# Kernel tuning notes

Hardware: AMD Instinct MI355X
Metric: run time of the kernel (lower is better)

The kernel has to match this reference:

```python
import jax, jax.numpy as jnp
import numpy as np

B, N, C_IN = 8, 8192, 64
M, K, RADIUS = 1024, 64, 0.2   # num_centers, num_neighbors, ball radius
LAYERS = [128, 128, 256]
EPS = 1e-5


def setup_inputs() -> dict:
    key = jax.random.key(0)
    ks = jax.random.split(key, 3 + len(LAYERS))
    feat = jax.random.normal(ks[0], (B, C_IN, N), jnp.float32)
    coords = jax.random.uniform(ks[1], (B, 3, N), jnp.float32)  # unit cube
    cond = jax.random.normal(ks[2], (B, C_IN), jnp.float32)
    params = {}
    c_prev = C_IN + 3  # include_coordinates=True
    for i, c_out in enumerate(LAYERS):
        params[f"w{i}"] = jax.random.normal(ks[3 + i], (c_out, c_prev), jnp.float32) / np.sqrt(c_prev).astype(np.float32)
        params[f"b{i}"] = jnp.zeros((c_out,), jnp.float32)
        params[f"gamma{i}"] = jnp.ones((c_out,), jnp.float32)
        params[f"beta{i}"] = jnp.zeros((c_out,), jnp.float32)
        c_prev = c_out
    return {"feat": feat, "coords": coords, "cond": cond, **params}


def fps(pts, m):
    """Furthest point sampling. pts: (B,N,3) -> (B,m) int32 indices. Starts at index 0."""
    B_, N_, _ = pts.shape

    def step(carry, _):
        dist, far = carry                                   # (B,N), (B,)
        centroid = jnp.take_along_axis(pts, far[:, None, None], axis=1)  # (B,1,3)
        d = jnp.sum((pts - centroid) ** 2, -1)              # (B,N)
        dist = jnp.minimum(dist, d)
        nxt = jnp.argmax(dist, -1).astype(jnp.int32)
        return (dist, nxt), far

    init = (jnp.full((B_, N_), 1e10, jnp.float32), jnp.zeros((B_,), jnp.int32))
    _, idx = jax.lax.scan(step, init, None, length=m)
    return idx.T                                            # (B,m)


def ball_query(pts, centers, radius, k):
    """pts (B,N,3), centers (B,M,3) -> neighbor indices (B,M,k).
    First k in-radius points (original order); empty slots repeat the first hit."""
    d2 = jnp.sum((centers[:, :, None, :] - pts[:, None, :, :]) ** 2, -1)  # (B,M,N)
    within = d2 < radius * radius
    # stable sort keys: valid points (0) first, keeping original point order
    order = jnp.argsort(jnp.where(within, 0, 1).astype(jnp.int32), axis=-1, stable=True)[..., :k]
    cnt = within.sum(-1, keepdims=True)                      # (B,M,1)
    slot = jnp.arange(k)
    return jnp.where(slot < cnt, order, order[..., :1])      # pad with first valid idx


def gather(x, idx):
    """x (B,N,D), idx (B,M,K) -> (B,M,K,D)"""
    return jax.vmap(lambda a, i: a[i])(x, idx)


def reference(feat, coords, cond,
              w0, b0, gamma0, beta0,
              w1, b1, gamma1, beta1,
              w2, b2, gamma2, beta2):
    pts = coords.transpose(0, 2, 1)                          # (B,N,3)
    cidx = fps(pts, M)                                       # (B,M)
    centers = jnp.take_along_axis(pts, cidx[..., None], axis=1)  # (B,M,3)
    nidx = ball_query(pts, centers, RADIUS, K)               # (B,M,K)
    rel = gather(pts, nidx) - centers[:, :, None, :]         # (B,M,K,3) relative coords
    nfeat = gather(feat.transpose(0, 2, 1), nidx)            # (B,M,K,C)
    x = jnp.concatenate([rel, nfeat], axis=-1)               # (B,M,K,3+C), coords first
    # Shared MLP: 1x1 conv + BatchNorm (batch stats) + ReLU per layer
    for w, b, g, be in ((w0, b0, gamma0, beta0), (w1, b1, gamma1, beta1), (w2, b2, gamma2, beta2)):
        x = jnp.einsum('bmkc,oc->bmko', x, w) + b
        mu = x.mean((0, 1, 2))
        var = x.var((0, 1, 2))
        x = (x - mu) * jax.lax.rsqrt(var + EPS) * g + be
        x = jax.nn.relu(x)
    out = x.max(axis=2).transpose(0, 2, 1)                   # max over nsample -> (B,Cout,M)
    return out, centers.transpose(0, 2, 1), cond
```

## Files before the change

### kernel.cpp

```cpp
#include <hip/hip_runtime.h>

#define NB    8
#define NPTS  8192
#define NCTR  1024
#define KNN   64
#define NGRP  8192
#define SAMP  524288
#define EPSB  1e-5f

#define OFF_CIDX 0ull
#define OFF_NIDX 32768ull
#define OFF_SS   2129920ull
#define OFF_PSUM 2134016ull
#define OFF_PSQR 4231168ull
#define OFF_GMAX 6328320ull
#define OFF_GMIN 14716928ull
#define OFF_FT   23105536ull
#define OFF_Y1   31494144ull
#define NEED_BIG 165711872ull

typedef unsigned short ushort8 __attribute__((ext_vector_type(8)));
typedef short short8v __attribute__((ext_vector_type(8)));
typedef float f32x4 __attribute__((ext_vector_type(4)));
typedef float f32x2 __attribute__((ext_vector_type(2)));

__device__ __forceinline__ unsigned short f2b(float f) {
  unsigned int u = __builtin_bit_cast(unsigned int, f);
  u += 0x7fffu + ((u >> 16) & 1u);
  return (unsigned short)(u >> 16);
}
__device__ __forceinline__ float b2f(unsigned short s) {
  unsigned int u = ((unsigned int)s) << 16;
  return __builtin_bit_cast(float, u);
}

template <int CTRL>
__device__ __forceinline__ float dppmax(float x) {
  int m = __builtin_amdgcn_update_dpp(0, __builtin_bit_cast(int, x), CTRL, 0xf, 0xf, true);
  return fmaxf(x, __builtin_bit_cast(float, m));
}

__global__ __launch_bounds__(256) void fps_kernel(const float* __restrict__ coords,
                                                  int* __restrict__ cidx,
                                                  float* __restrict__ centers_out) {
  const int b = blockIdx.x;
  const int t = threadIdx.x;
  const int wid = t >> 6, lane = t & 63;
  __shared__ float4 sc4[NPTS];
  __shared__ unsigned long long red[2][4];
  const float* cb = coords + (size_t)b * 3 * NPTS;
  for (int i = t; i < NPTS; i += 256)
    sc4[i] = make_float4(cb[i], cb[NPTS + i], cb[2 * NPTS + i], 0.f);
  __syncthreads();
  constexpr int PT = NPTS / 256;
  constexpr int P2 = PT / 2;
  f32x2 px[P2], py[P2], pz[P2], dst[P2];
#pragma unroll
  for (int j = 0; j < P2; ++j) {
    int p = t * PT + 2 * j;
    px[j] = (f32x2){cb[p], cb[p + 1]};
    py[j] = (f32x2){cb[NPTS + p], cb[NPTS + p + 1]};
    pz[j] = (f32x2){cb[2 * NPTS + p], cb[2 * NPTS + p + 1]};
    dst[j] = (f32x2){1e10f, 1e10f};
  }
  int cur = 0;
  float4 c0 = sc4[0];
  float cx = c0.x, cy = c0.y, cz = c0.z;
  int parity = 0;
  for (int s = 0; s < NCTR; ++s) {
    if (t == 0) {
      cidx[b * NCTR + s] = cur;
      centers_out[(b * 3 + 0) * NCTR + s] = cx;
      centers_out[(b * 3 + 1) * NCTR + s] = cy;
      centers_out[(b * 3 + 2) * NCTR + s] = cz;
    }
    f32x2 cx2 = {cx, cx}, cy2 = {cy, cy}, cz2 = {cz, cz};
    f32x2 bv2 = {-1.0f, -1.0f};
#pragma unroll
    for (int j = 0; j < P2; ++j) {
#pragma clang fp contract(off)
      f32x2 dx = px[j] - cx2;
      f32x2 dy = py[j] - cy2;
      f32x2 dz = pz[j] - cz2;
      f32x2 d2 = (dx * dx + dy * dy) + dz * dz;
      f32x2 nd = __builtin_elementwise_min(dst[j], d2);
      dst[j] = nd;
      bv2 = __builtin_elementwise_max(bv2, nd);
    }
    float bv = fmaxf(bv2.x, bv2.y);
    float r = bv;
    r = dppmax<0x111>(r);
    r = dppmax<0x112>(r);
    r = dppmax<0x114>(r);
    r = dppmax<0x118>(r);
    r = dppmax<0x142>(r);
    r = dppmax<0x143>(r);
    float wm = __builtin_bit_cast(float,
        __builtin_amdgcn_readlane(__builtin_bit_cast(int, r), 63));
    int li = 0x7fffffff;
#pragma unroll
    for (int j = P2 - 1; j >= 0; --j) {
      if (dst[j].y == wm) li = t * PT + 2 * j + 1;
      if (dst[j].x == wm) li = t * PT + 2 * j;
    }
    unsigned long long mask = __ballot(bv == wm);
    int widx = __shfl(li, (int)__builtin_ctzll(mask));
    if (lane == 0)
      red[parity][wid] =
          ((unsigned long long)__builtin_bit_cast(unsigned int, wm) << 32) |
          (unsigned long long)(~(unsigned int)widx);
    __syncthreads();
    unsigned long long best = red[parity][0];
#pragma unroll
    for (int k = 1; k < 4; ++k) {
      unsigned long long o = red[parity][k];
      best = (o > best) ? o : best;
    }
    cur = (int)(~(unsigned int)best);
    float4 cc = sc4[cur];
    cx = cc.x; cy = cc.y; cz = cc.z;
    parity ^= 1;
  }
}

__global__ __launch_bounds__(256) void featT_kernel(const float* __restrict__ feat,
                                                    unsigned short* __restrict__ fT) {
  int b  = blockIdx.y;
  int j  = blockIdx.x * 64 + (threadIdx.x & 63);
  int cg = threadIdx.x >> 6;
  ushort8 v0, v1;
#pragma unroll
  for (int cc = 0; cc < 8; ++cc)
    v0[cc] = f2b(feat[((size_t)b * 64 + cg * 16 + cc) * NPTS + j]);
#pragma unroll
  for (int cc = 0; cc < 8; ++cc)
    v1[cc] = f2b(feat[((size_t)b * 64 + cg * 16 + 8 + cc) * NPTS + j]);
  unsigned short* dst = fT + ((size_t)b * NPTS + j) * 64 + cg * 16;
  *(ushort8*)dst = v0;
  *(ushort8*)(dst + 8) = v1;
}

__global__ __launch_bounds__(256) void bq_kernel(const float* __restrict__ coords,
                                                 const int* __restrict__ cidx,
                                                 int* __restrict__ nidx) {
  const int b = blockIdx.y;
  const int w = threadIdx.x >> 6, lane = threadIdx.x & 63;
  const int m = blockIdx.x * 4 + w;
  const float* cb = coords + (size_t)b * 3 * NPTS;
  const int cen = cidx[b * NCTR + m];
  const float cx = cb[cen], cy = cb[NPTS + cen], cz = cb[2 * NPTS + cen];
  int* outp = nidx + ((size_t)b * NCTR + m) * KNN;
  const float RR = (float)(0.2 * 0.2);
  int found = 0, first = -1;
  for (int chunk = 0; chunk < NPTS / 64 && found < KNN; ++chunk) {
    int p = chunk * 64 + lane;
    float dx = __fsub_rn(cx, cb[p]);
    float dy = __fsub_rn(cy, cb[NPTS + p]);
    float dz = __fsub_rn(cz, cb[2 * NPTS + p]);
    float d2 = __fadd_rn(__fadd_rn(__fmul_rn(dx, dx), __fmul_rn(dy, dy)), __fmul_rn(dz, dz));
    bool pred = d2 < RR;
    unsigned long long mask = __ballot(pred);
    if (pred) {
      int rank = __popcll(mask & ((1ull << lane) - 1ull));
      int slot = found + rank;
      if (slot < KNN) outp[slot] = p;
    }
    if (first < 0 && mask != 0ull) first = chunk * 64 + __builtin_ctzll(mask);
    found += __popcll(mask);
  }
  if (found < KNN) {
    int f = (first < 0) ? 0 : first;
    if (lane >= found) outp[lane] = f;
  }
}

template <int NL, bool READY1, bool WRITEY1>
__global__ __launch_bounds__(256) void fused_kernel(
    const unsigned short* __restrict__ fT, const float* __restrict__ coords,
    const int* __restrict__ cidx, const int* __restrict__ nidx,
    unsigned short* __restrict__ y1, const float* __restrict__ ss,
    const float* __restrict__ w0, const float* __restrict__ b0,
    const float* __restrict__ w1, const float* __restrict__ b1,
    const float* __restrict__ w2, const float* __restrict__ b2,
    float* __restrict__ psum, float* __restrict__ psqr,
    float* __restrict__ gmax, float* __restrict__ gmin) {
  __shared__ __align__(16) unsigned short Xs[4 * 64 * 128];
  __shared__ __align__(16) unsigned short Wbuf[128 * 128];
  __shared__ float s_bias[128];
  __shared__ float s_sc0[128], s_sh0[128], s_sc1[128], s_sh1[128];
  __shared__ float s_rs[4][128], s_rq[4][128];

  const int t = threadIdx.x;
  const int wg = t >> 6, lane = t & 63;
  const int r16 = lane & 15, kg = lane >> 4;
  const int g = blockIdx.x * 4 + wg;
  const int bb_ = g >> 10;
  const int rsw = lane & 7;
  unsigned short* xrow = &Xs[(wg * 64 + lane) * 128];

  if constexpr (NL >= 2 && !READY1) {
    if (t < 128) { s_sc0[t] = ss[t]; s_sh0[t] = ss[128 + t]; }
  }
  if constexpr (NL >= 3) {
    if (t < 128) { s_sc1[t] = ss[256 + t]; s_sh1[t] = ss[384 + t]; }
  }

  auto stageW = [&](const float* w, const float* bia, bool remap0, int oh) {
    for (int e = t; e < 128 * 128; e += 256) {
      int o = e >> 7, c = e & 127;
      float v;
      if (remap0) {
        int lc = (c < 64) ? (c + 3) : ((c < 67) ? (c - 64) : -1);
        v = (lc >= 0) ? w[o * 67 + lc] : 0.f;
      } else {
        v = w[((size_t)(oh * 128 + o)) * 128 + c];
      }
      Wbuf[(o << 7) + ((((c >> 3) ^ (o & 7)) << 3) | (c & 7))] = f2b(v);
    }
    if (t < 128) s_bias[t] = bia[oh * 128 + t];
  };

  auto statsOut = [&](float (&sv8)[8], float (&sq8)[8], int coff) {
#pragma unroll
    for (int nt = 0; nt < 8; ++nt) {
      sv8[nt] += __shfl_xor(sv8[nt], 16); sv8[nt] += __shfl_xor(sv8[nt], 32);
      sq8[nt] += __shfl_xor(sq8[nt], 16); sq8[nt] += __shfl_xor(sq8[nt], 32);
    }
    if (lane < 16) {
#pragma unroll
      for (int nt = 0; nt < 8; ++nt) {
        s_rs[wg][nt * 16 + lane] = sv8[nt];
        s_rq[wg][nt * 16 + lane] = sq8[nt];
      }
    }
    __syncthreads();
    if (t < 128) {
      float sB = s_rs[0][t] + s_rs[1][t] + s_rs[2][t] + s_rs[3][t];
      float qB = s_rq[0][t] + s_rq[1][t] + s_rq[2][t] + s_rq[3][t];
      psum[(size_t)blockIdx.x * 256 + coff + t] = sB;
      psqr[(size_t)blockIdx.x * 256 + coff + t] = qB;
    }
  };

  short8v a[4][4];

  if constexpr (!READY1) {
    {
      int j = nidx[(size_t)g * KNN + lane];
      int cen = cidx[g];
      const unsigned short* fr = fT + ((size_t)bb_ * NPTS + j) * 64;
#pragma unroll
      for (int ch = 0; ch < 8; ++ch)
        *(ushort8*)(xrow + ((ch ^ rsw) << 3)) = *(const ushort8*)(fr + ch * 8);
      const float* cb = coords + (size_t)bb_ * 3 * NPTS;
      float rx = __fsub_rn(cb[j], cb[cen]);
      float ry = __fsub_rn(cb[NPTS + j], cb[NPTS + cen]);
      float rz = __fsub_rn(cb[2 * NPTS + j], cb[2 * NPTS + cen]);
      ushort8 rv = {f2b(rx), f2b(ry), f2b(rz), 0, 0, 0, 0, 0};
      *(ushort8*)(xrow + ((8 ^ rsw) << 3)) = rv;
      ushort8 zz = {0, 0, 0, 0, 0, 0, 0, 0};
#pragma unroll
      for (int ch = 9; ch < 16; ++ch)
        *(ushort8*)(xrow + ((ch ^ rsw) << 3)) = zz;
    }
    stageW(w0, b0, true, 0);
    __syncthreads();

#pragma unroll
    for (int st = 0; st < 4; ++st) {
      int row = st * 16 + r16;
#pragma unroll
      for (int ks = 0; ks < 3; ++ks)
        a[st][ks] = __builtin_bit_cast(short8v,
            *(const ushort8*)&Xs[(wg * 64 + row) * 128 + (((ks * 4 + kg) ^ (row & 7)) << 3)]);
    }
    {
      float sv8[8], sq8[8];
#pragma unroll
      for (int nt = 0; nt < 8; ++nt) { sv8[nt] = 0.f; sq8[nt] = 0.f; }
#pragma unroll
      for (int nt = 0; nt < 8; ++nt) {
        int o = nt * 16 + r16;
        short8v wb[3];
#pragma unroll
        for (int ks = 0; ks < 3; ++ks)
          wb[ks] = __builtin_bit_cast(short8v,
              *(const ushort8*)&Wbuf[(o << 7) + (((ks * 4 + kg) ^ (o & 7)) << 3)]);
        float bia = s_bias[o];
        float sc = 0.f, sh = 0.f;
        if constexpr (NL >= 2) { sc = s_sc0[o]; sh = s_sh0[o]; }
#pragma unroll
        for (int st = 0; st < 4; ++st) {
          f32x4 acc = {0.f, 0.f, 0.f, 0.f};
#pragma unroll
          for (int ks = 0; ks < 3; ++ks)
            acc = __builtin_amdgcn_mfma_f32_16x16x32_bf16(a[st][ks], wb[ks], acc, 0, 0, 0);
#pragma unroll
          for (int r = 0; r < 4; ++r) {
            float v = acc[r] + bia;
            if constexpr (NL == 1) {
              sv8[nt] += v; sq8[nt] = fmaf(v, v, sq8[nt]);
            } else {
              float x = fmaxf(fmaf(v, sc, sh), 0.f);
              int row = st * 16 + kg * 4 + r;
              Xs[(wg * 64 + row) * 128 + ((((o >> 3) ^ (row & 7)) << 3) | (o & 7))] = f2b(x);
            }
          }
        }
      }
      if constexpr (NL == 1) { statsOut(sv8, sq8, 0); return; }
    }

    if constexpr (NL >= 2) {
      __syncthreads();
      stageW(w1, b1, false, 0);
      __syncthreads();
#pragma unroll
    for (int st = 0; st < 4; ++st) {
        int row = st * 16 + r16;
#pragma unroll
        for (int ks = 0; ks < 4; ++ks)
          a[st][ks] = __builtin_bit_cast(short8v,
              *(const ushort8*)&Xs[(wg * 64 + row) * 128 + (((ks * 4 + kg) ^ (row & 7)) << 3)]);
      }
      float sv8[8], sq8[8];
#pragma unroll
      for (int nt = 0; nt < 8; ++nt) { sv8[nt] = 0.f; sq8[nt] = 0.f; }
#pragma unroll
      for (int nt = 0; nt < 8; ++nt) {
        int o = nt * 16 + r16;
        short8v wb[4];
#pragma unroll
        for (int ks = 0; ks < 4; ++ks)
          wb[ks] = __builtin_bit_cast(short8v,
              *(const ushort8*)&Wbuf[(o << 7) + (((ks * 4 + kg) ^ (o & 7)) << 3)]);
        float bia = s_bias[o];
        float sc = 0.f, sh = 0.f;
        if constexpr (NL >= 3) { sc = s_sc1[o]; sh = s_sh1[o]; }
#pragma unroll
        for (int st = 0; st < 4; ++st) {
          f32x4 acc = {0.f, 0.f, 0.f, 0.f};
#pragma unroll
          for (int ks = 0; ks < 4; ++ks)
            acc = __builtin_amdgcn_mfma_f32_16x16x32_bf16(a[st][ks], wb[ks], acc, 0, 0, 0);
#pragma unroll
          for (int r = 0; r < 4; ++r) {
            float v = acc[r] + bia;
            int row = st * 16 + kg * 4 + r;
            if constexpr (NL == 2) {
              sv8[nt] += v; sq8[nt] = fmaf(v, v, sq8[nt]);
              if constexpr (WRITEY1)
                y1[((size_t)g * 64 + row) * 128 + o] = f2b(v);
            } else {
              float x = fmaxf(fmaf(v, sc, sh), 0.f);
              Xs[(wg * 64 + row) * 128 + ((((o >> 3) ^ (row & 7)) << 3) | (o & 7))] = f2b(x);
            }
          }
        }
      }
      if constexpr (NL == 2) { statsOut(sv8, sq8, 0); return; }
    }
  } else {
    __syncthreads();
    const unsigned short* yr = y1 + ((size_t)g * 64 + lane) * 128;
#pragma unroll
    for (int ch = 0; ch < 16; ++ch) {
      ushort8 vv = *(const ushort8*)(yr + ch * 8);
      ushort8 ov;
#pragma unroll
      for (int jj = 0; jj < 8; ++jj) {
        int c = ch * 8 + jj;
        ov[jj] = f2b(fmaxf(fmaf(b2f(vv[jj]), s_sc1[c], s_sh1[c]), 0.f));
      }
      *(ushort8*)(xrow + ((ch ^ rsw) << 3)) = ov;
    }
  }

  if constexpr (NL == 3) {
#pragma unroll
    for (int st = 0; st < 4; ++st) {
      int row = st * 16 + r16;
#pragma unroll
      for (int ks = 0; ks < 4; ++ks)
        a[st][ks] = __builtin_bit_cast(short8v,
            *(const ushort8*)&Xs[(wg * 64 + row) * 128 + (((ks * 4 + kg) ^ (row & 7)) << 3)]);
    }
    for (int h = 0; h < 2; ++h) {
      __syncthreads();
      stageW(w2, b2, false, h);
      __syncthreads();
      float mx8[8], mn8[8], sv8[8], sq8[8];
#pragma unroll
      for (int nt = 0; nt < 8; ++nt) { mx8[nt] = -1e30f; mn8[nt] = 1e30f; sv8[nt] = 0.f; sq8[nt] = 0.f; }
#pragma unroll
      for (int nt = 0; nt < 8; ++nt) {
        int o = nt * 16 + r16;
        short8v wb[4];
#pragma unroll
        for (int ks = 0; ks < 4; ++ks)
          wb[ks] = __builtin_bit_cast(short8v,
              *(const ushort8*)&Wbuf[(o << 7) + (((ks * 4 + kg) ^ (o & 7)) << 3)]);
        float bia = s_bias[o];
#pragma unroll
        for (int st = 0; st < 4; ++st) {
          f32x4 acc = {0.f, 0.f, 0.f, 0.f};
#pragma unroll
          for (int ks = 0; ks < 4; ++ks)
            acc = __builtin_amdgcn_mfma_f32_16x16x32_bf16(a[st][ks], wb[ks], acc, 0, 0, 0);
#pragma unroll
          for (int r = 0; r < 4; ++r) {
            float v = acc[r] + bia;
            mx8[nt] = fmaxf(mx8[nt], v); mn8[nt] = fminf(mn8[nt], v);
            sv8[nt] += v; sq8[nt] = fmaf(v, v, sq8[nt]);
          }
        }
      }
#pragma unroll
      for (int nt = 0; nt < 8; ++nt) {
        mx8[nt] = fmaxf(mx8[nt], __shfl_xor(mx8[nt], 16));
        mx8[nt] = fmaxf(mx8[nt], __shfl_xor(mx8[nt], 32));
        mn8[nt] = fminf(mn8[nt], __shfl_xor(mn8[nt], 16));
        mn8[nt] = fminf(mn8[nt], __shfl_xor(mn8[nt], 32));
      }
      if (lane < 16) {
#pragma unroll
        for (int nt = 0; nt < 8; ++nt) {
          gmax[(size_t)g * 256 + h * 128 + nt * 16 + lane] = mx8[nt];
          gmin[(size_t)g * 256 + h * 128 + nt * 16 + lane] = mn8[nt];
        }
      }
      statsOut(sv8, sq8, h * 128);
    }
  }
}

template <int O>
__global__ __launch_bounds__(256) void ss_kernel(const float* __restrict__ psum,
                                                 const float* __restrict__ psqr,
                                                 const float* __restrict__ gamma,
                                                 const float* __restrict__ beta,
                                                 float* __restrict__ ss_out) {
  int c = blockIdx.x;
  int t = threadIdx.x;
  float s = 0.f, q = 0.f;
  for (int i = t; i < 2048; i += 256) {
    s += psum[(size_t)i * 256 + c];
    q += psqr[(size_t)i * 256 + c];
  }
  int lane = t & 63, wid = t >> 6;
#pragma unroll
  for (int off = 32; off > 0; off >>= 1) { s += __shfl_down(s, off); q += __shfl_down(q, off); }
  __shared__ float rv[4], rqv[4];
  if (lane == 0) { rv[wid] = s; rqv[wid] = q; }
  __syncthreads();
  if (t == 0) {
    s = rv[0] + rv[1] + rv[2] + rv[3];
    q = rqv[0] + rqv[1] + rqv[2] + rqv[3];
    const float inv = 1.0f / (float)SAMP;
    float mu = s * inv;
    float var = fmaxf(q * inv - mu * mu, 0.f);
    float rs = 1.0f / sqrtf(var + EPSB);
    float sc = gamma[c] * rs;
    ss_out[c] = sc;
    ss_out[O + c] = beta[c] - mu * sc;
  }
}

__global__ __launch_bounds__(256) void final_kernel(const float* __restrict__ gmax,
                                                    const float* __restrict__ gmin,
                                                    const float* __restrict__ ss2,
                                                    float* __restrict__ out) {
  int b = blockIdx.x >> 5, mt = blockIdx.x & 31;
  int t = threadIdx.x;
  __shared__ float tile[32][257];
  float sc = ss2[t], sh = ss2[256 + t];
  size_t base = ((size_t)b * 1024 + mt * 32) * 256;
#pragma unroll
  for (int r = 0; r < 32; ++r) {
    float A = fmaf(gmax[base + r * 256 + t], sc, sh);
    float C = fmaf(gmin[base + r * 256 + t], sc, sh);
    tile[r][t] = fmaxf(fmaxf(A, C), 0.f);
  }
  __syncthreads();
  for (int i = t; i < 8192; i += 256) {
    int o = i >> 5, ml = i & 31;
    out[((size_t)b * 256 + o) * 1024 + mt * 32 + ml] = tile[ml][o];
  }
}

__global__ void cond_kernel(const float* __restrict__ cond, float* __restrict__ dst) {
  dst[threadIdx.x] = cond[threadIdx.x];
}

extern "C" void kernel_launch(void* const* d_in, const int* in_sizes, int n_in,
                              void* d_out, int out_size, void* d_ws, size_t ws_size,
                              hipStream_t stream) {
  const float* feat   = (const float*)d_in[0];
  const float* coords = (const float*)d_in[1];
  const float* cond   = (const float*)d_in[2];
  const float* w0  = (const float*)d_in[3];
  const float* b0  = (const float*)d_in[4];
  const float* ga0 = (const float*)d_in[5];
  const float* be0 = (const float*)d_in[6];
  const float* w1  = (const float*)d_in[7];
  const float* b1  = (const float*)d_in[8];
  const float* ga1 = (const float*)d_in[9];
  const float* be1 = (const float*)d_in[10];
  const float* w2  = (const float*)d_in[11];
  const float* b2  = (const float*)d_in[12];
  const float* ga2 = (const float*)d_in[13];
  const float* be2 = (const float*)d_in[14];

  char* ws = (char*)d_ws;
  int* cidxp = (int*)(ws + OFF_CIDX);
  int* nidxp = (int*)(ws + OFF_NIDX);
  float* ss   = (float*)(ws + OFF_SS);
  float* psum = (float*)(ws + OFF_PSUM);
  float* psqr = (float*)(ws + OFF_PSQR);
  float* gmax = (float*)(ws + OFF_GMAX);
  float* gmin = (float*)(ws + OFF_GMIN);
  unsigned short* fT = (unsigned short*)(ws + OFF_FT);
  unsigned short* y1 = (unsigned short*)(ws + OFF_Y1);

  float* out         = (float*)d_out;
  float* centers_out = out + (size_t)8 * 256 * 1024;
  float* cond_out    = centers_out + (size_t)8 * 3 * 1024;

  const bool big = (ws_size >= NEED_BIG);

  fps_kernel<<<8, 256, 0, stream>>>(coords, cidxp, centers_out);
  featT_kernel<<<dim3(128, 8), 256, 0, stream>>>(feat, fT);
  bq_kernel<<<dim3(256, 8), 256, 0, stream>>>(coords, cidxp, nidxp);

  fused_kernel<1, false, false><<<2048, 256, 0, stream>>>(
      fT, coords, cidxp, nidxp, y1, ss, w0, b0, w1, b1, w2, b2, psum, psqr, gmax, gmin);
  ss_kernel<128><<<128, 256, 0, stream>>>(psum, psqr, ga0, be0, ss);

  if (big) {
    fused_kernel<2, false, true><<<2048, 256, 0, stream>>>(
        fT, coords, cidxp, nidxp, y1, ss, w0, b0, w1, b1, w2, b2, psum, psqr, gmax, gmin);
  } else {
    fused_kernel<2, false, false><<<2048, 256, 0, stream>>>(
        fT, coords, cidxp, nidxp, y1, ss, w0, b0, w1, b1, w2, b2, psum, psqr, gmax, gmin);
  }
  ss_kernel<128><<<128, 256, 0, stream>>>(psum, psqr, ga1, be1, ss + 256);

  if (big) {
    fused_kernel<3, true, false><<<2048, 256, 0, stream>>>(
        fT, coords, cidxp, nidxp, y1, ss, w0, b0, w1, b1, w2, b2, psum, psqr, gmax, gmin);
  } else {
    fused_kernel<3, false, false><<<2048, 256, 0, stream>>>(
        fT, coords, cidxp, nidxp, y1, ss, w0, b0, w1, b1, w2, b2, psum, psqr, gmax, gmin);
  }
  ss_kernel<256><<<256, 256, 0, stream>>>(psum, psqr, ga2, be2, ss + 512);

  final_kernel<<<256, 256, 0, stream>>>(gmax, gmin, ss + 512, out);
  cond_kernel<<<1, 512, 0, stream>>>(cond, cond_out);
}
```

Before: 1.504 ms.

## Spatially bin points in FPS so threads skip distance updates via bbox bound

Sorts each batch's points into an 8x8x8 voxel grid, using a shared-memory counting sort, so each thread owns a spatially compact set of 32 points with a bounding box. On every FPS step a thread compares the box's minimum distance to the new center with its current best min-distance and skips the distance update when no point can change. The per-wave argmax tie-break now goes through a packed original-index key reduced with DPP instead of ballot plus shuffle. This adds a sort prologue and some branch divergence, and relies on keeping the original index order for ties.

```diff
diff --git a/kernel.cpp b/kernel.cpp
--- a/kernel.cpp
+++ b/kernel.cpp
@@ -39,33 +39,90 @@
   int m = __builtin_amdgcn_update_dpp(0, __builtin_bit_cast(int, x), CTRL, 0xf, 0xf, true);
   return fmaxf(x, __builtin_bit_cast(float, m));
 }
+template <int CTRL>
+__device__ __forceinline__ unsigned dppumax(unsigned x) {
+  unsigned m = (unsigned)__builtin_amdgcn_update_dpp(0, (int)x, CTRL, 0xf, 0xf, true);
+  return (x > m) ? x : m;
+}
 
 __global__ __launch_bounds__(256) void fps_kernel(const float* __restrict__ coords,
                                                   int* __restrict__ cidx,
                                                   float* __restrict__ centers_out) {
-  const int b = blockIdx.x;
-  const int t = threadIdx.x;
+  const int b = blockIdx.x, t = threadIdx.x;
   const int wid = t >> 6, lane = t & 63;
-  __shared__ float4 sc4[NPTS];
+  __shared__ float4 pts[NPTS];
+  __shared__ int cnt[512];
+  __shared__ int part[256];
+  __shared__ int cstart[512];
   __shared__ unsigned long long red[2][4];
   const float* cb = coords + (size_t)b * 3 * NPTS;
-  for (int i = t; i < NPTS; i += 256)
-    sc4[i] = make_float4(cb[i], cb[NPTS + i], cb[2 * NPTS + i], 0.f);
-  __syncthreads();
-  constexpr int PT = NPTS / 256;
-  constexpr int P2 = PT / 2;
+
+  cnt[t] = 0; cnt[t + 256] = 0;
+  __syncthreads();
+  for (int i = t; i < NPTS; i += 256) {
+    float x = cb[i], y = cb[NPTS + i], z = cb[2 * NPTS + i];
+    int ix = min(max((int)(x * 8.f), 0), 7);
+    int iy = min(max((int)(y * 8.f), 0), 7);
+    int iz = min(max((int)(z * 8.f), 0), 7);
+    atomicAdd(&cnt[ix + 8 * iy + 64 * iz], 1);
+  }
+  __syncthreads();
+  part[t] = cnt[2 * t] + cnt[2 * t + 1];
+  __syncthreads();
+  for (int off = 1; off < 256; off <<= 1) {
+    int v = (t >= off) ? part[t - off] : 0;
+    __syncthreads();
+    part[t] += v;
+    __syncthreads();
+  }
+  {
+    int e = (t > 0) ? part[t - 1] : 0;
+    cstart[2 * t] = e;
+    cstart[2 * t + 1] = e + cnt[2 * t];
+  }
+  __syncthreads();
+  cnt[t] = 0; cnt[t + 256] = 0;
+  __syncthreads();
+  for (int i = t; i < NPTS; i += 256) {
+    float x = cb[i], y = cb[NPTS + i], z = cb[2 * NPTS + i];
+    int ix = min(max((int)(x * 8.f), 0), 7);
+    int iy = min(max((int)(y * 8.f), 0), 7);
+    int iz = min(max((int)(z * 8.f), 0), 7);
+    int c = ix + 8 * iy + 64 * iz;
+    int r = atomicAdd(&cnt[c], 1);
+    int slot = cstart[c] + r;
+    pts[slot] = make_float4(x, y, z, __builtin_bit_cast(float, i));
+  }
+  __syncthreads();
+
+  constexpr int PT = 32, P2 = 16;
   f32x2 px[P2], py[P2], pz[P2], dst[P2];
+  unsigned noi[PT];
+  float lox = 1e30f, loy = 1e30f, loz = 1e30f;
+  float hix = -1e30f, hiy = -1e30f, hiz = -1e30f;
 #pragma unroll
   for (int j = 0; j < P2; ++j) {
-    int p = t * PT + 2 * j;
-    px[j] = (f32x2){cb[p], cb[p + 1]};
-    py[j] = (f32x2){cb[NPTS + p], cb[NPTS + p + 1]};
-    pz[j] = (f32x2){cb[2 * NPTS + p], cb[2 * NPTS + p + 1]};
+    int s0 = t * PT + 2 * j;
+    float4 p0 = pts[s0];
+    float4 p1 = pts[s0 + 1];
+    px[j] = (f32x2){p0.x, p1.x};
+    py[j] = (f32x2){p0.y, p1.y};
+    pz[j] = (f32x2){p0.z, p1.z};
     dst[j] = (f32x2){1e10f, 1e10f};
-  }
+    lox = fminf(lox, fminf(p0.x, p1.x)); hix = fmaxf(hix, fmaxf(p0.x, p1.x));
+    loy = fminf(loy, fminf(p0.y, p1.y)); hiy = fmaxf(hiy, fmaxf(p0.y, p1.y));
+    loz = fminf(loz, fminf(p0.z, p1.z)); hiz = fmaxf(hiz, fmaxf(p0.z, p1.z));
+    noi[2 * j]     = (((8191u - (unsigned)__builtin_bit_cast(int, p0.w)) << 13) | (unsigned)s0) + 1u;
+    noi[2 * j + 1] = (((8191u - (unsigned)__builtin_bit_cast(int, p1.w)) << 13) | (unsigned)(s0 + 1)) + 1u;
+  }
+  unsigned bl0 = 0;
+#pragma unroll
+  for (int k = 0; k < PT; ++k) bl0 = (noi[k] > bl0) ? noi[k] : bl0;
+  unsigned long long bestpk =
+      ((unsigned long long)(unsigned)__builtin_bit_cast(int, 1e10f) << 32) | bl0;
+
+  float cx = cb[0], cy = cb[NPTS], cz = cb[2 * NPTS];
   int cur = 0;
-  float4 c0 = sc4[0];
-  float cx = c0.x, cy = c0.y, cz = c0.z;
   int parity = 0;
   for (int s = 0; s < NCTR; ++s) {
     if (t == 0) {
@@ -74,20 +131,35 @@
       centers_out[(b * 3 + 1) * NCTR + s] = cy;
       centers_out[(b * 3 + 2) * NCTR + s] = cz;
     }
-    f32x2 cx2 = {cx, cx}, cy2 = {cy, cy}, cz2 = {cz, cz};
-    f32x2 bv2 = {-1.0f, -1.0f};
-#pragma unroll
-    for (int j = 0; j < P2; ++j) {
+    float gx = fmaxf(fmaxf(lox - cx, cx - hix), 0.f);
+    float gy = fmaxf(fmaxf(loy - cy, cy - hiy), 0.f);
+    float gz = fmaxf(fmaxf(loz - cz, cz - hiz), 0.f);
+    float d2m = gx * gx + gy * gy + gz * gz;
+    float bval = __builtin_bit_cast(float, (unsigned)(bestpk >> 32));
+    if (d2m * 0.9999f < bval) {
+      f32x2 cx2 = {cx, cx}, cy2 = {cy, cy}, cz2 = {cz, cz};
+      f32x2 bv2 = {-1.0f, -1.0f};
+#pragma unroll
+      for (int j = 0; j < P2; ++j) {
 #pragma clang fp contract(off)
-      f32x2 dx = px[j] - cx2;
-      f32x2 dy = py[j] - cy2;
-      f32x2 dz = pz[j] - cz2;
-      f32x2 d2 = (dx * dx + dy * dy) + dz * dz;
-      f32x2 nd = __builtin_elementwise_min(dst[j], d2);
-      dst[j] = nd;
-      bv2 = __builtin_elementwise_max(bv2, nd);
-    }
-    float bv = fmaxf(bv2.x, bv2.y);
+        f32x2 dx = px[j] - cx2;
+        f32x2 dy = py[j] - cy2;
+        f32x2 dz = pz[j] - cz2;
+        f32x2 d2 = (dx * dx + dy * dy) + dz * dz;
+        f32x2 nd = __builtin_elementwise_min(dst[j], d2);
+        dst[j] = nd;
+        bv2 = __builtin_elementwise_max(bv2, nd);
+      }
+      float bv = fmaxf(bv2.x, bv2.y);
+      unsigned low = 0;
+#pragma unroll
+      for (int j = 0; j < P2; ++j) {
+        if (dst[j].x == bv && noi[2 * j] > low) low = noi[2 * j];
+        if (dst[j].y == bv && noi[2 * j + 1] > low) low = noi[2 * j + 1];
+      }
+      bestpk = ((unsigned long long)(unsigned)__builtin_bit_cast(int, bv) << 32) | low;
+    }
+    float bv = __builtin_bit_cast(float, (unsigned)(bestpk >> 32));
     float r = bv;
     r = dppmax<0x111>(r);
     r = dppmax<0x112>(r);
@@ -97,18 +169,17 @@
     r = dppmax<0x143>(r);
     float wm = __builtin_bit_cast(float,
         __builtin_amdgcn_readlane(__builtin_bit_cast(int, r), 63));
-    int li = 0x7fffffff;
-#pragma unroll
-    for (int j = P2 - 1; j >= 0; --j) {
-      if (dst[j].y == wm) li = t * PT + 2 * j + 1;
-      if (dst[j].x == wm) li = t * PT + 2 * j;
-    }
-    unsigned long long mask = __ballot(bv == wm);
-    int widx = __shfl(li, (int)__builtin_ctzll(mask));
+    unsigned cl = (bv == wm) ? (unsigned)bestpk : 0u;
+    cl = dppumax<0x111>(cl);
+    cl = dppumax<0x112>(cl);
+    cl = dppumax<0x114>(cl);
+    cl = dppumax<0x118>(cl);
+    cl = dppumax<0x142>(cl);
+    cl = dppumax<0x143>(cl);
+    unsigned um = (unsigned)__builtin_amdgcn_readlane((int)cl, 63);
     if (lane == 0)
       red[parity][wid] =
-          ((unsigned long long)__builtin_bit_cast(unsigned int, wm) << 32) |
-          (unsigned long long)(~(unsigned int)widx);
+          ((unsigned long long)(unsigned)__builtin_bit_cast(int, wm) << 32) | um;
     __syncthreads();
     unsigned long long best = red[parity][0];
 #pragma unroll
@@ -116,8 +187,10 @@
       unsigned long long o = red[parity][k];
       best = (o > best) ? o : best;
     }
-    cur = (int)(~(unsigned int)best);
-    float4 cc = sc4[cur];
+    unsigned low = (unsigned)best - 1u;
+    int slot = (int)(low & 8191u);
+    cur = 8191 - (int)(low >> 13);
+    float4 cc = pts[slot];
     cx = cc.x; cy = cc.y; cz = cc.z;
     parity ^= 1;
   }
```

Measured after the change: 1.972 ms. 1.31x slower.
